# Kernel optimization log

Hardware: AMD Instinct MI355X
Metric: run time of the kernel (lower is better)

The kernel has to match this reference:

```python
import jax, jax.numpy as jnp
import numpy as np

B, N, D, K = 4, 4096, 2048, 4  # batch, seq_len, hidden_size, conv_kernel


def setup_inputs() -> dict:
    key = jax.random.key(0)
    k1, k2, k3 = jax.random.split(key, 3)
    x = jax.random.normal(k1, (B, N, D), dtype=jnp.float32)
    conv_weight = jax.random.normal(k2, (D, K), dtype=jnp.float32) * 0.1  # depthwise weight [D, K]
    conv_bias = jax.random.normal(k3, (D,), dtype=jnp.float32) * 0.1
    return {"x": x, "conv_weight": conv_weight, "conv_bias": conv_bias}


def reference(x, conv_weight, conv_bias):
    # Prefill path of TTTConv: depthwise causal conv1d + cache-state extraction.
    Bx, Nx, Dx = x.shape
    Kx = conv_weight.shape[1]
    xt = jnp.transpose(x, (0, 2, 1))  # [B, D, N]
    kernel = conv_weight[:, None, :]  # [D, 1, K] (O, I/groups, K)
    y = jax.lax.conv_general_dilated(
        xt, kernel,
        window_strides=(1,),
        padding=[(Kx - 1, 0)],  # causal left pad only (causal_conv1d_fn semantics)
        dimension_numbers=("NCH", "OIH", "NCH"),
        feature_group_count=Dx,
    )
    y = y + conv_bias[None, :, None]
    conv_output = jnp.transpose(y, (0, 2, 1))  # [B, N, D]
    # cache state: F.pad(x^T, (K - N, 0)) with N >= K crops to the last K timesteps
    conv_states = xt[:, :, Nx - Kx:]  # [B, D, K]
    return conv_output, conv_states
```

## Files before the change

kernel.cpp:

```cpp
#include <hip/hip_runtime.h>


constexpr int B = 4, N = 4096, D = 2048, K = 4;
constexpr int T = 8;
constexpr int BLK = 256;
constexpr int DV = D / 4;
constexpr int DBLKS = DV / BLK;
constexpr int NCHUNKS = N / T;
constexpr int NWG = B * NCHUNKS * DBLKS;

__global__ __launch_bounds__(BLK, 2) void tttconv_main(
    const float* __restrict__ x, const float* __restrict__ w,
    const float* __restrict__ bias, float* __restrict__ out,
    float* __restrict__ st)
{
    int bid = blockIdx.x;
    int b = bid / (NCHUNKS * DBLKS);
    int rem = bid % (NCHUNKS * DBLKS);
    int nchunk = rem / DBLKS;
    int dblk = rem % DBLKS;
    int dv = dblk * BLK + threadIdx.x;
    int d = dv * 4;
    int n0 = nchunk * T;

    const float4* w4 = (const float4*)(w + (size_t)d * K);
    float4 wr0 = w4[0];
    float4 wr1 = w4[1];
    float4 wr2 = w4[2];
    float4 wr3 = w4[3];
    float4 bv = *(const float4*)(bias + d);

    const float* xbase = x + ((size_t)b * N) * D + d;
    float4 xin[T + K - 1];
    if (n0 >= K - 1) {
        #pragma unroll
        for (int j = 0; j < T + K - 1; ++j)
            xin[j] = *(const float4*)(xbase + (size_t)(n0 - (K - 1) + j) * D);
    } else {
        #pragma unroll
        for (int j = 0; j < T + K - 1; ++j) {
            int n = n0 - (K - 1) + j;
            xin[j] = (n >= 0) ? *(const float4*)(xbase + (size_t)n * D)
                              : make_float4(0.f, 0.f, 0.f, 0.f);
        }
    }

    float* obase = out + ((size_t)b * N) * D + d;
    #pragma unroll
    for (int t = 0; t < T; ++t) {
        float4 acc = bv;
        acc.x += wr0.x * xin[t + 0].x + wr0.y * xin[t + 1].x + wr0.z * xin[t + 2].x + wr0.w * xin[t + 3].x;
        acc.y += wr1.x * xin[t + 0].y + wr1.y * xin[t + 1].y + wr1.z * xin[t + 2].y + wr1.w * xin[t + 3].y;
        acc.z += wr2.x * xin[t + 0].z + wr2.y * xin[t + 1].z + wr2.z * xin[t + 2].z + wr2.w * xin[t + 3].z;
        acc.w += wr3.x * xin[t + 0].w + wr3.y * xin[t + 1].w + wr3.z * xin[t + 2].w + wr3.w * xin[t + 3].w;
        *(float4*)(obase + (size_t)(n0 + t) * D) = acc;
    }

    if (nchunk == NCHUNKS - 1) {
        float* sbase = st + ((size_t)b * D + d) * K;
        float4 s0 = make_float4(xin[T - 1].x, xin[T].x, xin[T + 1].x, xin[T + 2].x);
        float4 s1 = make_float4(xin[T - 1].y, xin[T].y, xin[T + 1].y, xin[T + 2].y);
        float4 s2 = make_float4(xin[T - 1].z, xin[T].z, xin[T + 1].z, xin[T + 2].z);
        float4 s3 = make_float4(xin[T - 1].w, xin[T].w, xin[T + 1].w, xin[T + 2].w);
        *(float4*)(sbase + 0 * K) = s0;
        *(float4*)(sbase + 1 * K) = s1;
        *(float4*)(sbase + 2 * K) = s2;
        *(float4*)(sbase + 3 * K) = s3;
    }
}

extern "C" void kernel_launch(void* const* d_in, const int* in_sizes, int n_in,
                              void* d_out, int out_size, void* d_ws, size_t ws_size,
                              hipStream_t stream)
{
    const float* x    = (const float*)d_in[0];
    const float* w    = (const float*)d_in[1];
    const float* bias = (const float*)d_in[2];
    float* out = (float*)d_out;
    float* st  = out + (size_t)B * N * D;

    tttconv_main<<<NWG, BLK, 0, stream>>>(x, w, bias, out, st);
}
```

Before: 232.2 us.

## Process longer time strips per thread with register ring-buffer prefetch

Each thread now covers a 32-row strip instead of an 8-row chunk. Input rows sit in a 16-entry register ring buffer, with loads issued 8 rows ahead of compute. This cuts the 3-row halo re-read overhead and keeps global loads in flight while results are stored. The grid has four times fewer workgroups and occupancy is hinted up to 4, which may limit latency hiding if register pressure is high.

Result: slower. 238.8 us (+2.8%).

```diff
diff --git a/kernel.cpp b/kernel.cpp
--- a/kernel.cpp
+++ b/kernel.cpp
@@ -2,26 +2,27 @@
 
 
 constexpr int B = 4, N = 4096, D = 2048, K = 4;
-constexpr int T = 8;
 constexpr int BLK = 256;
-constexpr int DV = D / 4;
-constexpr int DBLKS = DV / BLK;
-constexpr int NCHUNKS = N / T;
-constexpr int NWG = B * NCHUNKS * DBLKS;
+constexpr int STRIP = 32;
+constexpr int PF = 8;
+constexpr int CB = 16;
+constexpr int DBLKS = 2;
+constexpr int NSTRIPS = N / STRIP;
+constexpr int NWG = B * NSTRIPS * DBLKS;
 
-__global__ __launch_bounds__(BLK, 2) void tttconv_main(
+__global__ __launch_bounds__(BLK, 4) void tttconv_main(
     const float* __restrict__ x, const float* __restrict__ w,
     const float* __restrict__ bias, float* __restrict__ out,
     float* __restrict__ st)
 {
     int bid = blockIdx.x;
-    int b = bid / (NCHUNKS * DBLKS);
-    int rem = bid % (NCHUNKS * DBLKS);
-    int nchunk = rem / DBLKS;
+    int b = bid / (NSTRIPS * DBLKS);
+    int rem = bid % (NSTRIPS * DBLKS);
+    int strip = rem / DBLKS;
     int dblk = rem % DBLKS;
     int dv = dblk * BLK + threadIdx.x;
     int d = dv * 4;
-    int n0 = nchunk * T;
+    int n0 = strip * STRIP;
 
     const float4* w4 = (const float4*)(w + (size_t)d * K);
     float4 wr0 = w4[0];
@@ -30,38 +31,52 @@
     float4 wr3 = w4[3];
     float4 bv = *(const float4*)(bias + d);
 
-    const float* xbase = x + ((size_t)b * N) * D + d;
-    float4 xin[T + K - 1];
-    if (n0 >= K - 1) {
-        #pragma unroll
-        for (int j = 0; j < T + K - 1; ++j)
-            xin[j] = *(const float4*)(xbase + (size_t)(n0 - (K - 1) + j) * D);
+    const float* xb = x + ((size_t)b * N) * D + d;
+    float*       ob = out + ((size_t)b * N) * D + d;
+
+    float4 cb[CB];
+    if (n0 == 0) {
+        cb[13] = cb[14] = cb[15] = make_float4(0.f, 0.f, 0.f, 0.f);
     } else {
-        #pragma unroll
-        for (int j = 0; j < T + K - 1; ++j) {
-            int n = n0 - (K - 1) + j;
-            xin[j] = (n >= 0) ? *(const float4*)(xbase + (size_t)n * D)
-                              : make_float4(0.f, 0.f, 0.f, 0.f);
-        }
+        cb[13] = *(const float4*)(xb + (size_t)(n0 - 3) * D);
+        cb[14] = *(const float4*)(xb + (size_t)(n0 - 2) * D);
+        cb[15] = *(const float4*)(xb + (size_t)(n0 - 1) * D);
+    }
+    #pragma unroll
+    for (int j = 0; j < PF; ++j)
+        cb[j] = *(const float4*)(xb + (size_t)(n0 + j) * D);
+
+    #define COMPUTE_ROW(i)                                                      \
+    {                                                                           \
+        const float4 x0 = cb[((i) + 13) & 15];                                  \
+        const float4 x1 = cb[((i) + 14) & 15];                                  \
+        const float4 x2 = cb[((i) + 15) & 15];                                  \
+        const float4 x3 = cb[(i) & 15];                                         \
+        float4 a = bv;                                                          \
+        a.x += wr0.x * x0.x + wr0.y * x1.x + wr0.z * x2.x + wr0.w * x3.x;       \
+        a.y += wr1.x * x0.y + wr1.y * x1.y + wr1.z * x2.y + wr1.w * x3.y;       \
+        a.z += wr2.x * x0.z + wr2.y * x1.z + wr2.z * x2.z + wr2.w * x3.z;       \
+        a.w += wr3.x * x0.w + wr3.y * x1.w + wr3.z * x2.w + wr3.w * x3.w;       \
+        *(float4*)(ob + (size_t)(n0 + (i)) * D) = a;                            \
     }
 
-    float* obase = out + ((size_t)b * N) * D + d;
     #pragma unroll
-    for (int t = 0; t < T; ++t) {
-        float4 acc = bv;
-        acc.x += wr0.x * xin[t + 0].x + wr0.y * xin[t + 1].x + wr0.z * xin[t + 2].x + wr0.w * xin[t + 3].x;
-        acc.y += wr1.x * xin[t + 0].y + wr1.y * xin[t + 1].y + wr1.z * xin[t + 2].y + wr1.w * xin[t + 3].y;
-        acc.z += wr2.x * xin[t + 0].z + wr2.y * xin[t + 1].z + wr2.z * xin[t + 2].z + wr2.w * xin[t + 3].z;
-        acc.w += wr3.x * xin[t + 0].w + wr3.y * xin[t + 1].w + wr3.z * xin[t + 2].w + wr3.w * xin[t + 3].w;
-        *(float4*)(obase + (size_t)(n0 + t) * D) = acc;
+    for (int i = 0; i < STRIP - PF; ++i) {
+        COMPUTE_ROW(i);
+        cb[(i + PF) & 15] = *(const float4*)(xb + (size_t)(n0 + i + PF) * D);
     }
+    #pragma unroll
+    for (int i = STRIP - PF; i < STRIP; ++i) {
+        COMPUTE_ROW(i);
+    }
+    #undef COMPUTE_ROW
 
-    if (nchunk == NCHUNKS - 1) {
+    if (strip == NSTRIPS - 1) {
         float* sbase = st + ((size_t)b * D + d) * K;
-        float4 s0 = make_float4(xin[T - 1].x, xin[T].x, xin[T + 1].x, xin[T + 2].x);
-        float4 s1 = make_float4(xin[T - 1].y, xin[T].y, xin[T + 1].y, xin[T + 2].y);
-        float4 s2 = make_float4(xin[T - 1].z, xin[T].z, xin[T + 1].z, xin[T + 2].z);
-        float4 s3 = make_float4(xin[T - 1].w, xin[T].w, xin[T + 1].w, xin[T + 2].w);
+        float4 s0 = make_float4(cb[12].x, cb[13].x, cb[14].x, cb[15].x);
+        float4 s1 = make_float4(cb[12].y, cb[13].y, cb[14].y, cb[15].y);
+        float4 s2 = make_float4(cb[12].z, cb[13].z, cb[14].z, cb[15].z);
+        float4 s3 = make_float4(cb[12].w, cb[13].w, cb[14].w, cb[15].w);
         *(float4*)(sbase + 0 * K) = s0;
         *(float4*)(sbase + 1 * K) = s1;
         *(float4*)(sbase + 2 * K) = s2;
```
